# Optimization experiments

Hardware: AMD Instinct MI355X
Metric: run time of the kernel (lower is better)

Reference implementation:

```python
import jax, jax.numpy as jnp
import numpy as np

B, F, D = 1024, 16, 64
P = F * (F - 1) // 2  # 120 field pairs


def setup_inputs() -> dict:
    key = jax.random.key(0)
    k1, k2, k3 = jax.random.split(key, 3)
    x = jax.random.normal(k1, (B, F, D), dtype=jnp.float32)
    # torch Linear weight layout: [out_features, in_features] = [D, D*D], one per pair
    W = jax.random.normal(k2, (P, D, D * D), dtype=jnp.float32) * (1.0 / np.sqrt(D * D))
    b = jax.random.normal(k3, (P, D), dtype=jnp.float32) * 0.01
    return {"x": x, "W": W, "b": b}


def reference(x, W, b):
    # x: [B, F, D]; W: [P, D, D*D]; b: [P, D]
    Bs, Fs, Ds = x.shape
    Ps = W.shape[0]
    ii, jj = np.triu_indices(Fs, k=1)  # pair order matches nested (i, j>i) loop
    xi = x[:, ii, :]  # [B, P, D] -> left vector of outer product
    xj = x[:, jj, :]  # [B, P, D] -> right vector
    # Flattened outer tmp[b, a*D + c] = xi[b,p,a] * xj[b,p,c];
    # Linear: out = tmp @ W^T + b. Reshape W to [P, D_out, a, c] and fuse,
    # never materializing the [B, P, D*D] outer-product tensor.
    W3 = W.reshape(Ps, Ds, Ds, Ds)
    out = jnp.einsum('bpa,bpc,pkac->bpk', xi, xj, W3) + b[None, :, :]
    return out  # [B, P, D]
```

## Files before the change

kernel.cpp:

```cpp
#include <hip/hip_runtime.h>
#include <stdint.h>
#include <stddef.h>

constexpr int NB = 1024;
constexpr int NF = 16;
constexpr int ND = 64;
constexpr int NP = 120;
constexpr int KD = ND * ND;
constexpr int OUT_STRIDE = NP * ND;

constexpr int BM = 256;
constexpr int NS = 32;

using floatx4  = __attribute__((ext_vector_type(4))) float;
using floatx16 = __attribute__((ext_vector_type(16))) float;
using half8    = __attribute__((ext_vector_type(8))) _Float16;
using half2v   = __attribute__((ext_vector_type(2))) _Float16;
using fp16x2   = __attribute__((ext_vector_type(2))) __fp16;
using uint4v   = __attribute__((ext_vector_type(4))) uint32_t;

constexpr int WCOL = ND * ND / 64 * 64;
constexpr int WSTG = 2 * WCOL;

__device__ __forceinline__ half2v pkh2(float f0, float f1) {
    fp16x2 h = __builtin_amdgcn_cvt_pkrtz(f0, f1);
    return __builtin_bit_cast(half2v, h);
}
__device__ __forceinline__ uint32_t pk16(float f0, float f1) {
    fp16x2 h = __builtin_amdgcn_cvt_pkrtz(f0, f1);
    return __builtin_bit_cast(uint32_t, h);
}
__device__ __forceinline__ uint16_t f16bits(float f) {
    return __builtin_bit_cast(uint16_t, (_Float16)f);
}

__device__ __forceinline__ void lds_barrier() {
    asm volatile("s_waitcnt lgkmcnt(0)" ::: "memory");
    __builtin_amdgcn_s_barrier();
    asm volatile("" ::: "memory");
}

__global__ __launch_bounds__(512, 4)
void outer_kernel(const float* __restrict__ x, const float* __restrict__ W,
                  const float* __restrict__ bias, float* __restrict__ out)
{
    __shared__ uint16_t lds_xit[ND * BM];
    __shared__ uint16_t lds_bt[2 * WSTG];

    const int p  = blockIdx.x;
    const int b0 = blockIdx.y * BM;

    int icol = 0, rem = p;
    while (rem >= NF - 1 - icol) { rem -= NF - 1 - icol; ++icol; }
    const int jcol = icol + 1 + rem;

    const int t    = threadIdx.x;
    const int wave = t >> 6;
    const int lane = t & 63;
    const int r32  = lane & 31;
    const int kh   = lane >> 5;
    const int wm   = wave & 3;
    const int wn   = wave >> 2;

    {
        const int mrow  = t >> 1;
        const int chalf = (t & 1) * 32;
        const int dbase = (mrow >> 6) * 64 + (mrow & 31) * 2 + ((mrow >> 5) & 1);
        const float* src = x + (size_t)(b0 + mrow) * (NF * ND) + icol * ND + chalf;
        #pragma unroll
        for (int c = 0; c < 32; c += 4) {
            floatx4 v = *(const floatx4*)(src + c);
            lds_xit[(chalf + c + 0) * BM + dbase] = f16bits(v.x);
            lds_xit[(chalf + c + 1) * BM + dbase] = f16bits(v.y);
            lds_xit[(chalf + c + 2) * BM + dbase] = f16bits(v.z);
            lds_xit[(chalf + c + 3) * BM + dbase] = f16bits(v.w);
        }
    }

    half2v xjh[2][16];
    #pragma unroll
    for (int mt = 0; mt < 2; ++mt) {
        const float* srow = x + (size_t)(b0 + wm*64 + mt*32 + r32) * (NF * ND)
                              + jcol * ND + kh * 8;
        #pragma unroll
        for (int kc = 0; kc < 4; ++kc) {
            floatx4 v0 = *(const floatx4*)(srow + kc * 16);
            floatx4 v1 = *(const floatx4*)(srow + kc * 16 + 4);
            xjh[mt][kc*4 + 0] = pkh2(v0.x, v0.y);
            xjh[mt][kc*4 + 1] = pkh2(v0.z, v0.w);
            xjh[mt][kc*4 + 2] = pkh2(v1.x, v1.y);
            xjh[mt][kc*4 + 3] = pkh2(v1.z, v1.w);
        }
    }

    const int n_st = t >> 3;
    const int cg   = t & 7;
    const float* wsrc = W + ((size_t)p * ND + n_st) * KD + cg * 8;
    uint16_t* bdst0 = &lds_bt[n_st * ND + ((cg ^ (n_st & 7)) * 8)];

    auto loadW2 = [&](int s2, floatx4* w) {
        const float* wp = wsrc + (size_t)(2 * s2) * ND;
        w[0] = *(const floatx4*)(wp);
        w[1] = *(const floatx4*)(wp + 4);
        w[2] = *(const floatx4*)(wp + ND);
        w[3] = *(const floatx4*)(wp + ND + 4);
    };
    auto packW2 = [&](int d, const floatx4* w) {
        #pragma unroll
        for (int sub = 0; sub < 2; ++sub) {
            uint16_t* bd = bdst0 + d * WSTG + sub * WCOL;
            uint4v q0 = (uint4v){ pk16(w[sub*2].x,   w[sub*2].y),   pk16(w[sub*2].z,   w[sub*2].w),
                                  pk16(w[sub*2+1].x, w[sub*2+1].y), pk16(w[sub*2+1].z, w[sub*2+1].w) };
            *(uint4v*)(bd) = q0;
        }
    };

    floatx16 acc[2] = {};

    const int nrow   = wn*32 + r32;
    const int bbase  = nrow * ND;
    const int bswz   = (r32 & 7);

    auto compute = [&](int s, int cur) {
        const int a0 = 2 * s;
        const uint16_t* rb = lds_bt + cur * WSTG;

        const uint32_t xi0 = *(const uint32_t*)&lds_xit[a0 * BM + wm*64 + r32*2];
        const uint32_t xi1 = *(const uint32_t*)&lds_xit[(a0 + 1) * BM + wm*64 + r32*2];
        const half2v xs00 = __builtin_bit_cast(half2v, __builtin_amdgcn_perm(xi0, xi0, 0x01000100u));
        const half2v xs01 = __builtin_bit_cast(half2v, __builtin_amdgcn_perm(xi0, xi0, 0x03020302u));
        const half2v xs10 = __builtin_bit_cast(half2v, __builtin_amdgcn_perm(xi1, xi1, 0x01000100u));
        const half2v xs11 = __builtin_bit_cast(half2v, __builtin_amdgcn_perm(xi1, xi1, 0x03020302u));

        __builtin_amdgcn_s_setprio(1);
        #pragma unroll
        for (int kc = 0; kc < 4; ++kc) {
            const int boff = bbase + (((2*kc + kh) ^ bswz) * 8);
            half8 bf0 = *(const half8*)&rb[boff];
            half8 bf1 = *(const half8*)&rb[WCOL + boff];

            union { half8 h8; half2v h2[4]; } a00, a01, a10, a11;
            #pragma unroll
            for (int q = 0; q < 4; ++q) {
                const half2v xv = xjh[0][kc*4 + q];
                const half2v yv = xjh[1][kc*4 + q];
                a00.h2[q] = xs00 * xv;
                a10.h2[q] = xs10 * xv;
                a01.h2[q] = xs01 * yv;
                a11.h2[q] = xs11 * yv;
            }
            acc[0] = __builtin_amdgcn_mfma_f32_32x32x16_f16(a00.h8, bf0, acc[0], 0, 0, 0);
            acc[1] = __builtin_amdgcn_mfma_f32_32x32x16_f16(a01.h8, bf0, acc[1], 0, 0, 0);
            acc[0] = __builtin_amdgcn_mfma_f32_32x32x16_f16(a10.h8, bf1, acc[0], 0, 0, 0);
            acc[1] = __builtin_amdgcn_mfma_f32_32x32x16_f16(a11.h8, bf1, acc[1], 0, 0, 0);
        }
        __builtin_amdgcn_s_setprio(0);
    };

    floatx4 wpk[4], wtmp[4];
    loadW2(0, wtmp);
    packW2(0, wtmp);
    loadW2(1, wpk);
    __syncthreads();

    #pragma unroll 1
    for (int s = 0; s < NS; ++s) {
        const int cur = s & 1;
        if (s + 1 < NS) packW2(cur ^ 1, wpk);
        if (s + 2 < NS) loadW2(s + 2, wpk);
        compute(s, cur);
        lds_barrier();
    }

    const float bb = bias[p * ND + wn*32 + r32];
    #pragma unroll
    for (int mt = 0; mt < 2; ++mt) {
        #pragma unroll
        for (int reg = 0; reg < 16; ++reg) {
            const int row = b0 + wm*64 + mt*32 + (reg & 3) + 8*(reg >> 2) + 4*kh;
            out[(size_t)row * OUT_STRIDE + p * ND + wn*32 + r32] = acc[mt][reg] + bb;
        }
    }
}

extern "C" void kernel_launch(void* const* d_in, const int* in_sizes, int n_in,
                              void* d_out, int out_size, void* d_ws, size_t ws_size,
                              hipStream_t stream) {
    const float* x    = (const float*)d_in[0];
    const float* W    = (const float*)d_in[1];
    const float* bias = (const float*)d_in[2];
    float* out = (float*)d_out;

    dim3 grid(NP, NB / BM);
    outer_kernel<<<grid, 512, 0, stream>>>(x, W, bias, out);
}
```

Measured before the change: 225.9 us.

## Split each W stage into two halves with extra barriers and new LDS layout

Changes the LDS layout of the staged fp16 W tile from a row-major XOR-swizzled form to a column-group-major layout, so each MFMA B-fragment is a contiguous per-lane read. Each stage now issues its global W load before the compute, reads half the B fragments up front, and interleaves the pack store for the next buffer between two half-stage MFMA groups. Extra barriers are added to keep waves in lockstep. The loop is unrolled by two with ping-pong register buffers. The aim is better overlap of global loads and LDS traffic with MFMA work, at the cost of more barriers per stage and possible bank conflicts from the unswizzled layout.

```diff
diff --git a/kernel.cpp b/kernel.cpp
--- a/kernel.cpp
+++ b/kernel.cpp
@@ -19,8 +19,7 @@
 using fp16x2   = __attribute__((ext_vector_type(2))) __fp16;
 using uint4v   = __attribute__((ext_vector_type(4))) uint32_t;
 
-constexpr int WCOL = ND * ND / 64 * 64;
-constexpr int WSTG = 2 * WCOL;
+constexpr int WBUF = 8192;
 
 __device__ __forceinline__ half2v pkh2(float f0, float f1) {
     fp16x2 h = __builtin_amdgcn_cvt_pkrtz(f0, f1);
@@ -33,9 +32,15 @@
 __device__ __forceinline__ uint16_t f16bits(float f) {
     return __builtin_bit_cast(uint16_t, (_Float16)f);
 }
-
-__device__ __forceinline__ void lds_barrier() {
+__device__ __forceinline__ half2v dupperm(uint32_t w, uint32_t sel) {
+    return __builtin_bit_cast(half2v, __builtin_amdgcn_perm(w, w, sel));
+}
+
+__device__ __forceinline__ void wait_lgkm0() {
     asm volatile("s_waitcnt lgkmcnt(0)" ::: "memory");
+}
+__device__ __forceinline__ void barrier_only() {
+    asm volatile("" ::: "memory");
     __builtin_amdgcn_s_barrier();
     asm volatile("" ::: "memory");
 }
@@ -45,7 +50,7 @@
                   const float* __restrict__ bias, float* __restrict__ out)
 {
     __shared__ uint16_t lds_xit[ND * BM];
-    __shared__ uint16_t lds_bt[2 * WSTG];
+    __shared__ uint16_t lds_w[2 * WBUF];
 
     const int p  = blockIdx.x;
     const int b0 = blockIdx.y * BM;
@@ -96,7 +101,7 @@
     const int n_st = t >> 3;
     const int cg   = t & 7;
     const float* wsrc = W + ((size_t)p * ND + n_st) * KD + cg * 8;
-    uint16_t* bdst0 = &lds_bt[n_st * ND + ((cg ^ (n_st & 7)) * 8)];
+    uint16_t* wdst = &lds_w[cg * 512 + n_st * 8];
 
     auto loadW2 = [&](int s2, floatx4* w) {
         const float* wp = wsrc + (size_t)(2 * s2) * ND;
@@ -105,71 +110,80 @@
         w[2] = *(const floatx4*)(wp + ND);
         w[3] = *(const floatx4*)(wp + ND + 4);
     };
-    auto packW2 = [&](int d, const floatx4* w) {
-        #pragma unroll
-        for (int sub = 0; sub < 2; ++sub) {
-            uint16_t* bd = bdst0 + d * WSTG + sub * WCOL;
-            uint4v q0 = (uint4v){ pk16(w[sub*2].x,   w[sub*2].y),   pk16(w[sub*2].z,   w[sub*2].w),
-                                  pk16(w[sub*2+1].x, w[sub*2+1].y), pk16(w[sub*2+1].z, w[sub*2+1].w) };
-            *(uint4v*)(bd) = q0;
+    auto packW2 = [&](int buf, const floatx4* w) {
+        #pragma unroll
+        for (int col = 0; col < 2; ++col) {
+            uint4v q = (uint4v){ pk16(w[col*2].x,   w[col*2].y),   pk16(w[col*2].z,   w[col*2].w),
+                                 pk16(w[col*2+1].x, w[col*2+1].y), pk16(w[col*2+1].z, w[col*2+1].w) };
+            *(uint4v*)(wdst + buf * WBUF + col * 4096) = q;
         }
     };
 
     floatx16 acc[2] = {};
-
-    const int nrow   = wn*32 + r32;
-    const int bbase  = nrow * ND;
-    const int bswz   = (r32 & 7);
-
-    auto compute = [&](int s, int cur) {
-        const int a0 = 2 * s;
-        const uint16_t* rb = lds_bt + cur * WSTG;
-
-        const uint32_t xi0 = *(const uint32_t*)&lds_xit[a0 * BM + wm*64 + r32*2];
-        const uint32_t xi1 = *(const uint32_t*)&lds_xit[(a0 + 1) * BM + wm*64 + r32*2];
-        const half2v xs00 = __builtin_bit_cast(half2v, __builtin_amdgcn_perm(xi0, xi0, 0x01000100u));
-        const half2v xs01 = __builtin_bit_cast(half2v, __builtin_amdgcn_perm(xi0, xi0, 0x03020302u));
-        const half2v xs10 = __builtin_bit_cast(half2v, __builtin_amdgcn_perm(xi1, xi1, 0x01000100u));
-        const half2v xs11 = __builtin_bit_cast(half2v, __builtin_amdgcn_perm(xi1, xi1, 0x03020302u));
-
-        __builtin_amdgcn_s_setprio(1);
-        #pragma unroll
-        for (int kc = 0; kc < 4; ++kc) {
-            const int boff = bbase + (((2*kc + kh) ^ bswz) * 8);
-            half8 bf0 = *(const half8*)&rb[boff];
-            half8 bf1 = *(const half8*)&rb[WCOL + boff];
-
-            union { half8 h8; half2v h2[4]; } a00, a01, a10, a11;
-            #pragma unroll
-            for (int q = 0; q < 4; ++q) {
-                const half2v xv = xjh[0][kc*4 + q];
-                const half2v yv = xjh[1][kc*4 + q];
-                a00.h2[q] = xs00 * xv;
-                a10.h2[q] = xs10 * xv;
-                a01.h2[q] = xs01 * yv;
-                a11.h2[q] = xs11 * yv;
-            }
-            acc[0] = __builtin_amdgcn_mfma_f32_32x32x16_f16(a00.h8, bf0, acc[0], 0, 0, 0);
-            acc[1] = __builtin_amdgcn_mfma_f32_32x32x16_f16(a01.h8, bf0, acc[1], 0, 0, 0);
-            acc[0] = __builtin_amdgcn_mfma_f32_32x32x16_f16(a10.h8, bf1, acc[0], 0, 0, 0);
-            acc[1] = __builtin_amdgcn_mfma_f32_32x32x16_f16(a11.h8, bf1, acc[1], 0, 0, 0);
-        }
-        __builtin_amdgcn_s_setprio(0);
-    };
-
-    floatx4 wpk[4], wtmp[4];
-    loadW2(0, wtmp);
-    packW2(0, wtmp);
-    loadW2(1, wpk);
+    const int rbase = kh * 512 + (wn * 32 + r32) * 8;
+
+#define MFMA4(kc_, bf0_, bf1_)                                                     \
+    {                                                                              \
+        union { half8 h8; half2v h2[4]; } a00, a01, a10, a11;                      \
+        _Pragma("unroll")                                                          \
+        for (int q = 0; q < 4; ++q) {                                              \
+            const half2v xv = xjh[0][(kc_)*4 + q];                                 \
+            const half2v yv = xjh[1][(kc_)*4 + q];                                 \
+            a00.h2[q] = xs00 * xv;  a10.h2[q] = xs10 * xv;                         \
+            a01.h2[q] = xs01 * yv;  a11.h2[q] = xs11 * yv;                         \
+        }                                                                          \
+        acc[0] = __builtin_amdgcn_mfma_f32_32x32x16_f16(a00.h8, bf0_, acc[0],0,0,0); \
+        acc[1] = __builtin_amdgcn_mfma_f32_32x32x16_f16(a01.h8, bf0_, acc[1],0,0,0); \
+        acc[0] = __builtin_amdgcn_mfma_f32_32x32x16_f16(a10.h8, bf1_, acc[0],0,0,0); \
+        acc[1] = __builtin_amdgcn_mfma_f32_32x32x16_f16(a11.h8, bf1_, acc[1],0,0,0); \
+    }
+
+#define STAGE(ss_, cur_, wload_, wpack_, doload_, dopack_)                         \
+    {                                                                              \
+        const int a0 = 2 * (ss_);                                                  \
+        const uint16_t* rb = lds_w + (cur_) * WBUF;                                \
+                          \
+        if (doload_) loadW2((ss_) + 2, wload_);                                    \
+        const uint32_t xi0 = *(const uint32_t*)&lds_xit[a0 * BM + wm*64 + r32*2];  \
+        const uint32_t xi1 = *(const uint32_t*)&lds_xit[(a0+1) * BM + wm*64 + r32*2]; \
+        half8 bA00 = *(const half8*)&rb[0*4096 + 0*1024 + rbase];                  \
+        half8 bA10 = *(const half8*)&rb[1*4096 + 0*1024 + rbase];                  \
+        half8 bA01 = *(const half8*)&rb[0*4096 + 1*1024 + rbase];                  \
+        half8 bA11 = *(const half8*)&rb[1*4096 + 1*1024 + rbase];                  \
+        const half2v xs00 = dupperm(xi0, 0x01000100u);                \
+        const half2v xs01 = dupperm(xi0, 0x03020302u);                \
+        const half2v xs10 = dupperm(xi1, 0x01000100u);                \
+        const half2v xs11 = dupperm(xi1, 0x03020302u);                \
+        barrier_only(); wait_lgkm0();                                              \
+        __builtin_amdgcn_s_setprio(1);                                             \
+        MFMA4(0, bA00, bA10);                                                      \
+        MFMA4(1, bA01, bA11);                                                      \
+        __builtin_amdgcn_s_setprio(0);                                             \
+        barrier_only();                                                            \
+                               \
+        half8 bB02 = *(const half8*)&rb[0*4096 + 2*1024 + rbase];                  \
+        half8 bB12 = *(const half8*)&rb[1*4096 + 2*1024 + rbase];                  \
+        half8 bB03 = *(const half8*)&rb[0*4096 + 3*1024 + rbase];                  \
+        half8 bB13 = *(const half8*)&rb[1*4096 + 3*1024 + rbase];                  \
+        if (dopack_) packW2((cur_) ^ 1, wpack_);                                   \
+        wait_lgkm0(); barrier_only();                                              \
+        __builtin_amdgcn_s_setprio(1);                                             \
+        MFMA4(2, bB02, bB12);                                                      \
+        MFMA4(3, bB03, bB13);                                                      \
+        __builtin_amdgcn_s_setprio(0);                                             \
+        barrier_only();                                                            \
+    }
+
+    floatx4 wr0[4], wr1[4];
+    loadW2(0, wr0);
+    packW2(0, wr0);
+    loadW2(1, wr0);
     __syncthreads();
 
     #pragma unroll 1
-    for (int s = 0; s < NS; ++s) {
-        const int cur = s & 1;
-        if (s + 1 < NS) packW2(cur ^ 1, wpk);
-        if (s + 2 < NS) loadW2(s + 2, wpk);
-        compute(s, cur);
-        lds_barrier();
+    for (int s = 0; s < NS; s += 2) {
+        STAGE(s,     0, wr1, wr0, (s + 2) < NS, true);
+        STAGE(s + 1, 1, wr0, wr1, (s + 3) < NS, (s + 2) < NS);
     }
 
     const float bb = bias[p * ND + wn*32 + r32];
@@ -181,6 +195,8 @@
             out[(size_t)row * OUT_STRIDE + p * ND + wn*32 + r32] = acc[mt][reg] + bb;
         }
     }
+#undef STAGE
+#undef MFMA4
 }
 
 extern "C" void kernel_launch(void* const* d_in, const int* in_sizes, int n_in,
```

After: 414.7 us. +83.5%, slower.
